# Kernel tuning notes

Measured on AMD Instinct MI355X. Metric: run time of the kernel, lower is better.

## Reference

```python
import jax, jax.numpy as jnp
import numpy as np

B, C, H, W = 8, 1024, 64, 64


def _conv(x, w, pad, dil=1):
    return jax.lax.conv_general_dilated(
        x, w, window_strides=(1, 1), padding=[(pad, pad), (pad, pad)],
        rhs_dilation=(dil, dil), dimension_numbers=("NCHW", "OIHW", "NCHW"))


def _gate(x, w0, w1, ws, bs):
    # LSK_AttentionGate_Strip: k_list=[5,7], d_list=[1,3]
    u1 = _conv(x, w0, 2, 1)                    # 5x5, pad 2
    u2 = _conv(u1, w1, 9, 3)                   # 7x7, dil 3, pad 9
    uc = jnp.concatenate([u1, u2], axis=1)     # [B,2,h,w]
    sa_avg = jnp.mean(uc, axis=1, keepdims=True)
    sa_max = jnp.max(uc, axis=1, keepdims=True)
    s = jnp.concatenate([sa_avg, sa_max], axis=1)
    attn = jax.nn.sigmoid(_conv(s, ws, 0, 1) + bs[None, :, None, None])
    res = u1 * attn[:, 0:1] + u2 * attn[:, 1:2]
    return jax.nn.sigmoid(res)


def setup_inputs() -> dict:
    key = jax.random.key(0)
    ks = jax.random.split(key, 20)
    d = {"x": jax.random.normal(ks[0], (B, C, H, W), dtype=jnp.float32)}
    names = ["h", "v", "d", "a"]
    for i, n in enumerate(names):
        k0, k1, k2, k3 = jax.random.split(ks[1 + i], 4)
        d[f"w{n}0"] = jax.random.normal(k0, (1, 1, 5, 5), dtype=jnp.float32) * 0.1
        d[f"w{n}1"] = jax.random.normal(k1, (1, 1, 7, 7), dtype=jnp.float32) * 0.1
        d[f"w{n}s"] = jax.random.normal(k2, (2, 2, 1, 1), dtype=jnp.float32) * 0.1
        d[f"b{n}s"] = jax.random.normal(k3, (2,), dtype=jnp.float32) * 0.1
    d["fusion_bias"] = jax.random.normal(ks[10], (1,), dtype=jnp.float32) * 0.1
    return d


def reference(x, wh0, wh1, whs, bhs, wv0, wv1, wvs, bvs,
              wd0, wd1, wds, bds, wa0, wa1, was, bas, fusion_bias):
    b, c, h, w = x.shape
    L = min(h, w)
    # horizontal / vertical strip contexts
    x_h = jnp.mean(jnp.mean(x, axis=3, keepdims=True), axis=1, keepdims=True)  # [B,1,H,1]
    attn_h = _gate(x_h, wh0, wh1, whs, bhs)
    x_v = jnp.mean(jnp.mean(x, axis=2, keepdims=True), axis=1, keepdims=True)  # [B,1,1,W]
    attn_v = _gate(x_v, wv0, wv1, wvs, bvs)
    # diagonal / anti-diagonal contexts
    raw_diag = jnp.diagonal(x, axis1=2, axis2=3)                 # [B,C,L]
    x_d = jnp.mean(raw_diag, axis=1, keepdims=True)[:, :, None, :]  # [B,1,1,L]
    attn_d = _gate(x_d, wd0, wd1, wds, bds)
    raw_anti = jnp.diagonal(x[..., ::-1], axis1=2, axis2=3)
    x_a = jnp.mean(raw_anti, axis=1, keepdims=True)[:, :, None, :]
    attn_a = _gate(x_a, wa0, wa1, was, bas)
    # project 1D gates onto 2D diagonals
    idx = jnp.arange(L)
    zeros = jnp.zeros((b, 1, h, w), dtype=x.dtype)
    map_d = zeros.at[:, :, idx, idx].set(attn_d[:, :, 0, :L])
    map_a = zeros.at[:, :, idx, idx[::-1]].set(attn_a[:, :, 0, :L])
    diag_context = map_d + map_a
    scale = 1.0 + fusion_bias * diag_context   # [B,1,H,W]
    out_h = x * attn_h * scale
    out_v = x * attn_v * scale
    return out_h, out_v
```

## Files before the change

kernel.cpp:

```cpp
#include <hip/hip_runtime.h>
#include <math.h>

#define NB 8
#define NC 1024
#define NH 64
#define NW 64
constexpr int PLANE = NH * NW;
constexpr long long NTOT = (long long)NB * NC * PLANE;


__global__ __launch_bounds__(256) void zero_kernel(float* ws) {
    int i = blockIdx.x * 256 + threadIdx.x;
    if (i < 2048) ws[i] = 0.0f;
}

__global__ __launch_bounds__(256) void reduce_kernel(const float* __restrict__ x,
                                                     float* __restrict__ gsum) {
    const int bid = blockIdx.x;
    const int b = bid >> 7;
    const int chunk = bid & 127;
    const int t = threadIdx.x;
    const int w0 = (t & 15) * 4;
    const int q  = t >> 4;

    const float* base = x + ((size_t)b * NC + (size_t)chunk * 8) * PLANE;

    float colacc0 = 0.f, colacc1 = 0.f, colacc2 = 0.f, colacc3 = 0.f;
    float rowacc[4] = {0.f, 0.f, 0.f, 0.f};
    float diagacc = 0.f, antiacc = 0.f;

    for (int c = 0; c < 8; ++c) {
        const float4* pl = (const float4*)(base + (size_t)c * PLANE);
        #pragma unroll
        for (int p = 0; p < 4; ++p) {
            float4 v = pl[p * 256 + t];
            colacc0 += v.x; colacc1 += v.y; colacc2 += v.z; colacc3 += v.w;
            rowacc[p] += v.x + v.y + v.z + v.w;
            int h = p * 16 + q;
            float dv = (h == w0)     ? v.x :
                       (h == w0 + 1) ? v.y :
                       (h == w0 + 2) ? v.z :
                       (h == w0 + 3) ? v.w : 0.f;
            diagacc += dv;
            int ac = 63 - h;
            float av = (ac == w0)     ? v.x :
                       (ac == w0 + 1) ? v.y :
                       (ac == w0 + 2) ? v.z :
                       (ac == w0 + 3) ? v.w : 0.f;
            antiacc += av;
        }
    }

    __shared__ float rowpart[4][256];
    __shared__ float colpart[256][4];
    __shared__ float sdiag[64];
    __shared__ float santi[64];

    #pragma unroll
    for (int p = 0; p < 4; ++p) rowpart[p][t] = rowacc[p];
    colpart[t][0] = colacc0; colpart[t][1] = colacc1;
    colpart[t][2] = colacc2; colpart[t][3] = colacc3;

    {
        int dj = (q - w0) & 15;
        if (dj < 4) sdiag[w0 + dj] = diagacc;
        int ak = (q - (60 - w0)) & 15;
        if (ak < 4) santi[60 - w0 + ak] = antiacc;
    }
    __syncthreads();

    if (t < 64) {
        int r = t;
        float s = 0.f;
        #pragma unroll
        for (int k = 0; k < 16; ++k) s += rowpart[r >> 4][(r & 15) * 16 + k];
        atomicAdd(gsum + b * 64 + r, s);
    } else if (t < 128) {
        int w = t - 64;
        float s = 0.f;
        #pragma unroll
        for (int k = 0; k < 16; ++k) s += colpart[(w >> 2) + k * 16][w & 3];
        atomicAdd(gsum + 512 + b * 64 + w, s);
    } else if (t < 192) {
        int r = t - 128;
        atomicAdd(gsum + 1024 + b * 64 + r, sdiag[r]);
    } else {
        int r = t - 192;
        atomicAdd(gsum + 1536 + b * 64 + r, santi[r]);
    }
}

struct GateW {
    const float* w0;
    const float* w1;
    const float* ws;
    const float* bs;
};

__device__ __forceinline__ float sigmoidf_(float v) {
    return 1.f / (1.f + expf(-v));
}

__global__ __launch_bounds__(256) void gate_kernel(const float* __restrict__ gsum,
                                                   GateW g0, GateW g1, GateW g2, GateW g3,
                                                   float* __restrict__ gates) {
    const int b = blockIdx.x;
    const int t = threadIdx.x;
    const int g = t >> 6;
    const int l = t & 63;

    GateW gw = (g == 0) ? g0 : (g == 1) ? g1 : (g == 2) ? g2 : g3;
    const float scale = (g < 2) ? (1.0f / 65536.0f) : (1.0f / 1024.0f);

    __shared__ float xm[4][64];
    __shared__ float u1s[4][64];

    xm[g][l] = gsum[g * 512 + b * 64 + l] * scale;
    __syncthreads();

    float u1v = 0.f;
    #pragma unroll
    for (int i = 0; i < 5; ++i) {
        float wv = gw.w0[(g == 0) ? (i * 5 + 2) : (10 + i)];
        int idx = l - 2 + i;
        if (idx >= 0 && idx < 64) u1v += xm[g][idx] * wv;
    }
    u1s[g][l] = u1v;
    __syncthreads();

    float u2v = 0.f;
    #pragma unroll
    for (int i = 0; i < 7; ++i) {
        float wv = gw.w1[(g == 0) ? (i * 7 + 3) : (21 + i)];
        int idx = l - 9 + 3 * i;
        if (idx >= 0 && idx < 64) u2v += u1s[g][idx] * wv;
    }

    float avg = 0.5f * (u1v + u2v);
    float mx  = fmaxf(u1v, u2v);
    float a0 = sigmoidf_(gw.ws[0] * avg + gw.ws[1] * mx + gw.bs[0]);
    float a1 = sigmoidf_(gw.ws[2] * avg + gw.ws[3] * mx + gw.bs[1]);
    float res = u1v * a0 + u2v * a1;
    gates[g * 512 + b * 64 + l] = sigmoidf_(res);
}

__global__ __launch_bounds__(256) void apply_kernel(const float* __restrict__ x,
                                                    const float* __restrict__ gates,
                                                    const float* __restrict__ fb_p,
                                                    float* __restrict__ out) {
    const float fb = fb_p[0];
    const size_t n4 = (size_t)NTOT / 4;
    const size_t stride = (size_t)gridDim.x * blockDim.x;
    const float4* x4 = (const float4*)x;
    float4* oh = (float4*)out;
    float4* ov = (float4*)(out + (size_t)NTOT);

    for (size_t i = (size_t)blockIdx.x * blockDim.x + threadIdx.x; i < n4; i += stride) {
        size_t e = i * 4;
        int w0 = (int)(e & 63);
        int h  = (int)((e >> 6) & 63);
        int b  = (int)(e >> 22);

        float4 v = x4[i];
        float ah = gates[b * 64 + h];
        float4 av = *(const float4*)(gates + 512 + b * 64 + w0);
        float gd = gates[1024 + b * 64 + h];
        float ga = gates[1536 + b * 64 + h];

        int hw = 63 - h;
        float sc0 = 1.f + fb * (((w0 + 0 == h) ? gd : 0.f) + ((w0 + 0 == hw) ? ga : 0.f));
        float sc1 = 1.f + fb * (((w0 + 1 == h) ? gd : 0.f) + ((w0 + 1 == hw) ? ga : 0.f));
        float sc2 = 1.f + fb * (((w0 + 2 == h) ? gd : 0.f) + ((w0 + 2 == hw) ? ga : 0.f));
        float sc3 = 1.f + fb * (((w0 + 3 == h) ? gd : 0.f) + ((w0 + 3 == hw) ? ga : 0.f));

        float4 o1, o2;
        o1.x = v.x * ah * sc0;  o1.y = v.y * ah * sc1;
        o1.z = v.z * ah * sc2;  o1.w = v.w * ah * sc3;
        o2.x = v.x * av.x * sc0; o2.y = v.y * av.y * sc1;
        o2.z = v.z * av.z * sc2; o2.w = v.w * av.w * sc3;

        oh[i] = o1;
        ov[i] = o2;
    }
}

extern "C" void kernel_launch(void* const* d_in, const int* in_sizes, int n_in,
                              void* d_out, int out_size, void* d_ws, size_t ws_size,
                              hipStream_t stream) {
    const float* x = (const float*)d_in[0];
    float* wsf = (float*)d_ws;

    GateW gh { (const float*)d_in[1],  (const float*)d_in[2],  (const float*)d_in[3],  (const float*)d_in[4]  };
    GateW gv { (const float*)d_in[5],  (const float*)d_in[6],  (const float*)d_in[7],  (const float*)d_in[8]  };
    GateW gd { (const float*)d_in[9],  (const float*)d_in[10], (const float*)d_in[11], (const float*)d_in[12] };
    GateW ga { (const float*)d_in[13], (const float*)d_in[14], (const float*)d_in[15], (const float*)d_in[16] };
    const float* fb = (const float*)d_in[17];

    zero_kernel<<<8, 256, 0, stream>>>(wsf);
    reduce_kernel<<<1024, 256, 0, stream>>>(x, wsf);
    gate_kernel<<<NB, 256, 0, stream>>>(wsf, gh, gv, gd, ga, wsf + 2048);
    apply_kernel<<<4096, 256, 0, stream>>>(x, wsf + 2048, fb, (float*)d_out);
}
```

Measured before the change: 429.0 us.

## Replace atomic reductions with per-block partials, drop zero kernel, nontemporal stores

The reduce kernel now runs 512 blocks, each covering 16 channel planes, and writes per-block partial sums to workspace instead of issuing atomicAdds. The gate kernel sums these partials itself, which removes the zero-init kernel launch and the atomic traffic. The apply kernel switches to 32-bit indexing and nontemporal stores for its two large output streams. In exchange, the gate kernel does a serial 64-way sum per thread, and the reduce kernel has fewer blocks to hide memory latency.

```diff
diff --git a/kernel.cpp b/kernel.cpp
--- a/kernel.cpp
+++ b/kernel.cpp
@@ -8,34 +8,35 @@
 constexpr int PLANE = NH * NW;
 constexpr long long NTOT = (long long)NB * NC * PLANE;
 
-
-__global__ __launch_bounds__(256) void zero_kernel(float* ws) {
-    int i = blockIdx.x * 256 + threadIdx.x;
-    if (i < 2048) ws[i] = 0.0f;
-}
+constexpr int RBLK = 512;
+constexpr int CHUNKS = RBLK / NB;
+constexpr int CPLANES = NC / CHUNKS;
+
+typedef float f4 __attribute__((ext_vector_type(4)));
+
 
 __global__ __launch_bounds__(256) void reduce_kernel(const float* __restrict__ x,
-                                                     float* __restrict__ gsum) {
+                                                     float* __restrict__ part) {
     const int bid = blockIdx.x;
-    const int b = bid >> 7;
-    const int chunk = bid & 127;
+    const int b = bid >> 6;
+    const int chunk = bid & 63;
     const int t = threadIdx.x;
     const int w0 = (t & 15) * 4;
     const int q  = t >> 4;
 
-    const float* base = x + ((size_t)b * NC + (size_t)chunk * 8) * PLANE;
+    const f4* base = (const f4*)(x + ((size_t)b * NC + (size_t)chunk * CPLANES) * PLANE);
 
     float colacc0 = 0.f, colacc1 = 0.f, colacc2 = 0.f, colacc3 = 0.f;
     float rowacc[4] = {0.f, 0.f, 0.f, 0.f};
     float diagacc = 0.f, antiacc = 0.f;
 
-    for (int c = 0; c < 8; ++c) {
-        const float4* pl = (const float4*)(base + (size_t)c * PLANE);
+    for (int c = 0; c < CPLANES; ++c) {
+        const f4* pl = base + (size_t)c * (PLANE / 4);
         #pragma unroll
         for (int p = 0; p < 4; ++p) {
-            float4 v = pl[p * 256 + t];
+            f4 v = pl[p * 256 + t];
             colacc0 += v.x; colacc1 += v.y; colacc2 += v.z; colacc3 += v.w;
-            rowacc[p] += v.x + v.y + v.z + v.w;
+            rowacc[p] += (v.x + v.y) + (v.z + v.w);
             int h = p * 16 + q;
             float dv = (h == w0)     ? v.x :
                        (h == w0 + 1) ? v.y :
@@ -69,24 +70,25 @@
     }
     __syncthreads();
 
+    float* outp = part + (size_t)bid * 256;
     if (t < 64) {
         int r = t;
         float s = 0.f;
         #pragma unroll
         for (int k = 0; k < 16; ++k) s += rowpart[r >> 4][(r & 15) * 16 + k];
-        atomicAdd(gsum + b * 64 + r, s);
+        outp[r] = s;
     } else if (t < 128) {
         int w = t - 64;
         float s = 0.f;
         #pragma unroll
         for (int k = 0; k < 16; ++k) s += colpart[(w >> 2) + k * 16][w & 3];
-        atomicAdd(gsum + 512 + b * 64 + w, s);
+        outp[64 + w] = s;
     } else if (t < 192) {
         int r = t - 128;
-        atomicAdd(gsum + 1024 + b * 64 + r, sdiag[r]);
+        outp[128 + r] = sdiag[r];
     } else {
         int r = t - 192;
-        atomicAdd(gsum + 1536 + b * 64 + r, santi[r]);
+        outp[192 + r] = santi[r];
     }
 }
 
@@ -101,7 +103,7 @@
     return 1.f / (1.f + expf(-v));
 }
 
-__global__ __launch_bounds__(256) void gate_kernel(const float* __restrict__ gsum,
+__global__ __launch_bounds__(256) void gate_kernel(const float* __restrict__ part,
                                                    GateW g0, GateW g1, GateW g2, GateW g3,
                                                    float* __restrict__ gates) {
     const int b = blockIdx.x;
@@ -115,7 +117,13 @@
     __shared__ float xm[4][64];
     __shared__ float u1s[4][64];
 
-    xm[g][l] = gsum[g * 512 + b * 64 + l] * scale;
+    {
+        const float* pp = part + (size_t)b * CHUNKS * 256 + g * 64 + l;
+        float s = 0.f;
+        #pragma unroll 8
+        for (int k = 0; k < CHUNKS; ++k) s += pp[(size_t)k * 256];
+        xm[g][l] = s * scale;
+    }
     __syncthreads();
 
     float u1v = 0.f;
@@ -149,21 +157,21 @@
                                                     const float* __restrict__ fb_p,
                                                     float* __restrict__ out) {
     const float fb = fb_p[0];
-    const size_t n4 = (size_t)NTOT / 4;
-    const size_t stride = (size_t)gridDim.x * blockDim.x;
-    const float4* x4 = (const float4*)x;
-    float4* oh = (float4*)out;
-    float4* ov = (float4*)(out + (size_t)NTOT);
-
-    for (size_t i = (size_t)blockIdx.x * blockDim.x + threadIdx.x; i < n4; i += stride) {
-        size_t e = i * 4;
+    const unsigned n4 = (unsigned)(NTOT / 4);
+    const unsigned stride = gridDim.x * blockDim.x;
+    const f4* x4 = (const f4*)x;
+    f4* oh = (f4*)out;
+    f4* ov = (f4*)(out + (size_t)NTOT);
+
+    for (unsigned i = blockIdx.x * blockDim.x + threadIdx.x; i < n4; i += stride) {
+        unsigned e = i * 4u;
         int w0 = (int)(e & 63);
         int h  = (int)((e >> 6) & 63);
         int b  = (int)(e >> 22);
 
-        float4 v = x4[i];
+        f4 v = x4[i];
         float ah = gates[b * 64 + h];
-        float4 av = *(const float4*)(gates + 512 + b * 64 + w0);
+        f4 av = *(const f4*)(gates + 512 + b * 64 + w0);
         float gd = gates[1024 + b * 64 + h];
         float ga = gates[1536 + b * 64 + h];
 
@@ -173,14 +181,14 @@
         float sc2 = 1.f + fb * (((w0 + 2 == h) ? gd : 0.f) + ((w0 + 2 == hw) ? ga : 0.f));
         float sc3 = 1.f + fb * (((w0 + 3 == h) ? gd : 0.f) + ((w0 + 3 == hw) ? ga : 0.f));
 
-        float4 o1, o2;
+        f4 o1, o2;
         o1.x = v.x * ah * sc0;  o1.y = v.y * ah * sc1;
         o1.z = v.z * ah * sc2;  o1.w = v.w * ah * sc3;
         o2.x = v.x * av.x * sc0; o2.y = v.y * av.y * sc1;
         o2.z = v.z * av.z * sc2; o2.w = v.w * av.w * sc3;
 
-        oh[i] = o1;
-        ov[i] = o2;
+        __builtin_nontemporal_store(o1, &oh[i]);
+        __builtin_nontemporal_store(o2, &ov[i]);
     }
 }
 
@@ -189,6 +197,8 @@
                               hipStream_t stream) {
     const float* x = (const float*)d_in[0];
     float* wsf = (float*)d_ws;
+    float* part = wsf;
+    float* gates = wsf + (size_t)RBLK * 256;
 
     GateW gh { (const float*)d_in[1],  (const float*)d_in[2],  (const float*)d_in[3],  (const float*)d_in[4]  };
     GateW gv { (const float*)d_in[5],  (const float*)d_in[6],  (const float*)d_in[7],  (const float*)d_in[8]  };
@@ -196,8 +206,7 @@
     GateW ga { (const float*)d_in[13], (const float*)d_in[14], (const float*)d_in[15], (const float*)d_in[16] };
     const float* fb = (const float*)d_in[17];
 
-    zero_kernel<<<8, 256, 0, stream>>>(wsf);
-    reduce_kernel<<<1024, 256, 0, stream>>>(x, wsf);
-    gate_kernel<<<NB, 256, 0, stream>>>(wsf, gh, gv, gd, ga, wsf + 2048);
-    apply_kernel<<<4096, 256, 0, stream>>>(x, wsf + 2048, fb, (float*)d_out);
-}
+    reduce_kernel<<<RBLK, 256, 0, stream>>>(x, part);
+    gate_kernel<<<NB, 256, 0, stream>>>(part, gh, gv, gd, ga, gates);
+    apply_kernel<<<4096, 256, 0, stream>>>(x, gates, fb, (float*)d_out);
+}
```

Measured after the change: 409.8 us. 1.05x faster.
